# Kernel optimization log

Measured on AMD Instinct MI355X. Metric: run time of the kernel, lower is better.

## Reference

```python
import jax, jax.numpy as jnp
import numpy as np

H, W, C = 64, 64, 2048
IMG = 224


def setup_inputs() -> dict:
    key = jax.random.key(0)
    features = jax.random.normal(key, (2, H, W, C), dtype=jnp.float32)
    return {"features": features, "img_size": IMG}


def reference(features, img_size):
    # features: [2, H, W, C] -- query (index 0) and target (index 1) feature maps.
    x0 = features[0]  # [H, W, C]
    x1 = features[1]  # [H, W, C]
    # Correlation volume: Decomposition[i,j,k,l] = sum_c x0[i,j,c] * x1[k,l,c]
    # (replaces the quadruple Python loop with a single GEMM-shaped einsum)
    decom = jnp.einsum('ijc,klc->ijkl', x0, x1)  # [H, W, H, W]
    decom = decom / jnp.max(decom)
    # NOTE: source calls `Decomposition.clamp(min=0)` without assignment -> no-op.
    decom_1 = jnp.sum(decom, axis=(2, 3))  # [H, W] saliency on query image
    decom_2 = jnp.sum(decom, axis=(0, 1))  # [H, W] saliency on target image
    stacked = jnp.stack((decom_1, decom_2))  # [2, H, W]
    # F.interpolate(mode='bilinear', align_corners=False) == half-pixel bilinear resize
    out = jax.image.resize(stacked, (2, img_size, img_size), method='bilinear')
    return out  # [2, img_size, img_size]
```

## Files before the change

kernel.cpp:

```cpp
#include <hip/hip_runtime.h>
#include <hip/hip_bf16.h>

#define HW    4096
#define CDIM  2048
#define IMG   224
#define NTKI  64
#define NTM   128
#define LROW  528
#define QSCALE 21.166666f

typedef int   int4v  __attribute__((ext_vector_type(4)));
typedef int   i32x16 __attribute__((ext_vector_type(16)));
typedef char  char4v __attribute__((ext_vector_type(4)));

__device__ __forceinline__ i32x16 zi16() {
    i32x16 z;
#pragma unroll
    for (int i = 0; i < 16; ++i) z[i] = 0;
    return z;
}
__device__ __forceinline__ char quant8(float x) {
    int r = __float2int_rn(x * QSCALE);
    r = min(max(r, -127), 127);
    return (char)r;
}

__global__ __launch_bounds__(256) void convert_pack_colsum(
    const float* __restrict__ feat,
    char* __restrict__ Ap, char* __restrict__ Bp,
    float* __restrict__ s0, float* __restrict__ s1) {
    __shared__ char lds[32 * LROW];
    __shared__ float csum[512];
    const int tid = threadIdx.x;
    const int mat = blockIdx.z;
    const int tm  = blockIdx.y;
    const int kb0 = blockIdx.x * 512;
    const float* src = feat + (size_t)mat * HW * CDIM + (size_t)(tm * 32) * CDIM + kb0;

    const int cc = (tid & 127) * 4;
    float a0 = 0.f, a1 = 0.f, a2 = 0.f, a3 = 0.f;
#pragma unroll
    for (int j = 0; j < 16; ++j) {
        const int r = j * 2 + (tid >> 7);
        float4 v = *(const float4*)&src[(size_t)r * CDIM + cc];
        a0 += v.x; a1 += v.y; a2 += v.z; a3 += v.w;
        char4v q;
        q[0] = quant8(v.x); q[1] = quant8(v.y);
        q[2] = quant8(v.z); q[3] = quant8(v.w);
        *(char4v*)&lds[r * LROW + cc] = q;
    }
    if (tid >= 128) {
        csum[cc + 0] = a0; csum[cc + 1] = a1;
        csum[cc + 2] = a2; csum[cc + 3] = a3;
    }
    __syncthreads();
    if (tid < 128) {
        float* s = mat ? s1 : s0;
        atomicAdd(&s[kb0 + cc + 0], a0 + csum[cc + 0]);
        atomicAdd(&s[kb0 + cc + 1], a1 + csum[cc + 1]);
        atomicAdd(&s[kb0 + cc + 2], a2 + csum[cc + 2]);
        atomicAdd(&s[kb0 + cc + 3], a3 + csum[cc + 3]);
    }

    const int l = tid & 63, w = tid >> 6;
    char* dstbase = mat ? Bp : Ap;
#pragma unroll
    for (int i = 0; i < 4; ++i) {
        const int tkl = w * 4 + i;
        int4v v = *(const int4v*)&lds[(l & 31) * LROW + tkl * 32 + (l >> 5) * 16];
        const int tkg = blockIdx.x * 16 + tkl;
        *(int4v*)&dstbase[((size_t)(tm * NTKI + tkg) * 64 + l) * 16] = v;
    }
}

__global__ __launch_bounds__(256, 4) void gemm_max_kernel(
    const char* __restrict__ Ap, const char* __restrict__ Bp,
    float* __restrict__ blockmax) {
    const int tid  = threadIdx.x;
    const int lane = tid & 63;
    const int wave = tid >> 6;
    const int wm = wave >> 1, wn = wave & 1;
    const int bm = blockIdx.y, bn = blockIdx.x;

    const int tmA = bm * 4 + wm * 2;
    const int tnB = bn * 4 + wn * 2;
    const char* a0p = Ap + (size_t)(tmA * NTKI) * 1024 + lane * 16;
    const char* a1p = a0p + (size_t)NTKI * 1024;
    const char* b0p = Bp + (size_t)(tnB * NTKI) * 1024 + lane * 16;
    const char* b1p = b0p + (size_t)NTKI * 1024;

    i32x16 acc00 = zi16(), acc01 = zi16(), acc10 = zi16(), acc11 = zi16();

    int4v ca0 = *(const int4v*)a0p;
    int4v ca1 = *(const int4v*)a1p;
    int4v cb0 = *(const int4v*)b0p;
    int4v cb1 = *(const int4v*)b1p;

#pragma unroll 2
    for (int tk = 0; tk < NTKI - 1; ++tk) {
        const size_t o = (size_t)(tk + 1) * 1024;
        const int4v na0 = *(const int4v*)(a0p + o);
        const int4v na1 = *(const int4v*)(a1p + o);
        const int4v nb0 = *(const int4v*)(b0p + o);
        const int4v nb1 = *(const int4v*)(b1p + o);
        acc00 = __builtin_amdgcn_mfma_i32_32x32x32_i8(ca0, cb0, acc00, 0, 0, 0);
        acc01 = __builtin_amdgcn_mfma_i32_32x32x32_i8(ca0, cb1, acc01, 0, 0, 0);
        acc10 = __builtin_amdgcn_mfma_i32_32x32x32_i8(ca1, cb0, acc10, 0, 0, 0);
        acc11 = __builtin_amdgcn_mfma_i32_32x32x32_i8(ca1, cb1, acc11, 0, 0, 0);
        ca0 = na0; ca1 = na1; cb0 = nb0; cb1 = nb1;
    }
    acc00 = __builtin_amdgcn_mfma_i32_32x32x32_i8(ca0, cb0, acc00, 0, 0, 0);
    acc01 = __builtin_amdgcn_mfma_i32_32x32x32_i8(ca0, cb1, acc01, 0, 0, 0);
    acc10 = __builtin_amdgcn_mfma_i32_32x32x32_i8(ca1, cb0, acc10, 0, 0, 0);
    acc11 = __builtin_amdgcn_mfma_i32_32x32x32_i8(ca1, cb1, acc11, 0, 0, 0);

    int m = INT_MIN;
#pragma unroll
    for (int i = 0; i < 16; ++i) {
        m = max(m, acc00[i]); m = max(m, acc01[i]);
        m = max(m, acc10[i]); m = max(m, acc11[i]);
    }
#pragma unroll
    for (int off = 32; off; off >>= 1)
        m = max(m, __shfl_down(m, off));

    __shared__ int wred[4];
    if (lane == 0) wred[wave] = m;
    __syncthreads();
    if (tid == 0) {
        const int im = max(max(wred[0], wred[1]), max(wred[2], wred[3]));
        blockmax[blockIdx.y * gridDim.x + blockIdx.x] =
            (float)im * (1.0f / (QSCALE * QSCALE));
    }
}

__global__ __launch_bounds__(256) void saliency_kernel(
    const float* __restrict__ feat, const float* __restrict__ s0,
    const float* __restrict__ s1, float* __restrict__ sal) {
    const int tid = threadIdx.x, lane = tid & 63, wave = tid >> 6;
    const int g = blockIdx.x * 4 + wave;
    const float* x;
    const float* s;
    if (g < HW) { x = feat + (size_t)g * CDIM;                            s = s1; }
    else        { x = feat + (size_t)HW * CDIM + (size_t)(g - HW) * CDIM; s = s0; }
    float acc = 0.f;
#pragma unroll
    for (int it = 0; it < 8; ++it) {
        const int c0 = it * 256 + lane * 4;
        float4 v = *(const float4*)&x[c0];
        float4 w = *(const float4*)&s[c0];
        acc += v.x * w.x + v.y * w.y + v.z * w.z + v.w * w.w;
    }
#pragma unroll
    for (int off = 32; off; off >>= 1) acc += __shfl_down(acc, off);
    if (lane == 0) sal[g] = acc;
}

__global__ __launch_bounds__(256) void resize_kernel(
    const float* __restrict__ sal, const float* __restrict__ bmax,
    float* __restrict__ out) {
    __shared__ float w[4];
    __shared__ float rM;
    const int tid = threadIdx.x;
    float m = -3.4e38f;
    for (int i = tid; i < 1024; i += 256) m = fmaxf(m, bmax[i]);
#pragma unroll
    for (int off = 32; off; off >>= 1) m = fmaxf(m, __shfl_down(m, off));
    if ((tid & 63) == 0) w[tid >> 6] = m;
    __syncthreads();
    if (tid == 0)
        rM = 1.0f / fmaxf(fmaxf(w[0], w[1]), fmaxf(w[2], w[3]));
    __syncthreads();

    const int idx = blockIdx.x * 256 + tid;
    if (idx >= 2 * IMG * IMG) return;
    const int ch = idx / (IMG * IMG);
    const int rem = idx % (IMG * IMG);
    const int oy = rem / IMG, ox = rem % IMG;
    const float scale = 64.0f / (float)IMG;
    const float sy = ((float)oy + 0.5f) * scale - 0.5f;
    const float sx = ((float)ox + 0.5f) * scale - 0.5f;
    const float fy0 = floorf(sy), fx0 = floorf(sx);
    const float wy = sy - fy0, wx = sx - fx0;
    int y0 = (int)fy0, x0 = (int)fx0;
    int y1 = min(max(y0 + 1, 0), 63), x1 = min(max(x0 + 1, 0), 63);
    y0 = min(max(y0, 0), 63); x0 = min(max(x0, 0), 63);
    const float* p = sal + ch * HW;
    const float v00 = p[y0 * 64 + x0], v01 = p[y0 * 64 + x1];
    const float v10 = p[y1 * 64 + x0], v11 = p[y1 * 64 + x1];
    out[idx] = ((1.f - wy) * ((1.f - wx) * v00 + wx * v01) +
                wy * ((1.f - wx) * v10 + wx * v11)) * rM;
}

extern "C" void kernel_launch(void* const* d_in, const int* in_sizes, int n_in,
                              void* d_out, int out_size, void* d_ws, size_t ws_size,
                              hipStream_t stream) {
    const float* feat = (const float*)d_in[0];
    float* out = (float*)d_out;

    char* ws = (char*)d_ws;
    char* Ap = ws;
    char* Bp = ws + (size_t)8 * 1024 * 1024;
    float* s0   = (float*)(ws + (size_t)16 * 1024 * 1024);
    float* s1   = s0 + CDIM;
    float* bmax = s1 + CDIM;
    float* sal  = bmax + 1024;

    hipMemsetAsync(s0, 0, 2 * CDIM * sizeof(float), stream);

    convert_pack_colsum<<<dim3(4, 128, 2), 256, 0, stream>>>(feat, Ap, Bp, s0, s1);
    gemm_max_kernel<<<dim3(32, 32), 256, 0, stream>>>(Ap, Bp, bmax);
    saliency_kernel<<<2048, 256, 0, stream>>>(feat, s0, s1, sal);
    const int nout = 2 * IMG * IMG;
    resize_kernel<<<(nout + 255) / 256, 256, 0, stream>>>(sal, bmax, out);
}
```

Measured before the change: 161.9 us.

## Replace atomic column sums with partials reduced inside GEMM kernel, drop memset

The convert kernel now handles 64 rows per block and writes per-block partial column sums to a buffer instead of using float atomics. The final 64-way reduction of those partials is folded into 16 blocks of the GEMM kernel. This removes the memset launch and the atomic contention. In exchange it doubles LDS use per convert block, halves that grid, and adds serial reduction work to a few GEMM blocks.

```diff
diff --git a/kernel.cpp b/kernel.cpp
--- a/kernel.cpp
+++ b/kernel.cpp
@@ -25,22 +25,22 @@
     return (char)r;
 }
 
-__global__ __launch_bounds__(256) void convert_pack_colsum(
+__global__ __launch_bounds__(256) void convert_pack_partial(
     const float* __restrict__ feat,
     char* __restrict__ Ap, char* __restrict__ Bp,
-    float* __restrict__ s0, float* __restrict__ s1) {
-    __shared__ char lds[32 * LROW];
+    float* __restrict__ P) {
+    __shared__ char lds[64 * LROW];
     __shared__ float csum[512];
     const int tid = threadIdx.x;
     const int mat = blockIdx.z;
-    const int tm  = blockIdx.y;
+    const int rm  = blockIdx.y;
     const int kb0 = blockIdx.x * 512;
-    const float* src = feat + (size_t)mat * HW * CDIM + (size_t)(tm * 32) * CDIM + kb0;
+    const float* src = feat + (size_t)mat * HW * CDIM + (size_t)(rm * 64) * CDIM + kb0;
 
     const int cc = (tid & 127) * 4;
     float a0 = 0.f, a1 = 0.f, a2 = 0.f, a3 = 0.f;
 #pragma unroll
-    for (int j = 0; j < 16; ++j) {
+    for (int j = 0; j < 32; ++j) {
         const int r = j * 2 + (tid >> 7);
         float4 v = *(const float4*)&src[(size_t)r * CDIM + cc];
         a0 += v.x; a1 += v.y; a2 += v.z; a3 += v.w;
@@ -55,19 +55,21 @@
     }
     __syncthreads();
     if (tid < 128) {
-        float* s = mat ? s1 : s0;
-        atomicAdd(&s[kb0 + cc + 0], a0 + csum[cc + 0]);
-        atomicAdd(&s[kb0 + cc + 1], a1 + csum[cc + 1]);
-        atomicAdd(&s[kb0 + cc + 2], a2 + csum[cc + 2]);
-        atomicAdd(&s[kb0 + cc + 3], a3 + csum[cc + 3]);
+        float4 p;
+        p.x = a0 + csum[cc + 0]; p.y = a1 + csum[cc + 1];
+        p.z = a2 + csum[cc + 2]; p.w = a3 + csum[cc + 3];
+        *(float4*)&P[((size_t)mat * 64 + rm) * CDIM + kb0 + cc] = p;
     }
 
     const int l = tid & 63, w = tid >> 6;
     char* dstbase = mat ? Bp : Ap;
 #pragma unroll
-    for (int i = 0; i < 4; ++i) {
-        const int tkl = w * 4 + i;
-        int4v v = *(const int4v*)&lds[(l & 31) * LROW + tkl * 32 + (l >> 5) * 16];
+    for (int i = 0; i < 8; ++i) {
+        const int t = w * 8 + i;
+        const int tml = t >> 4, tkl = t & 15;
+        int4v v = *(const int4v*)
+            &lds[(tml * 32 + (l & 31)) * LROW + tkl * 32 + (l >> 5) * 16];
+        const int tm  = rm * 2 + tml;
         const int tkg = blockIdx.x * 16 + tkl;
         *(int4v*)&dstbase[((size_t)(tm * NTKI + tkg) * 64 + l) * 16] = v;
     }
@@ -75,12 +77,23 @@
 
 __global__ __launch_bounds__(256, 4) void gemm_max_kernel(
     const char* __restrict__ Ap, const char* __restrict__ Bp,
+    const float* __restrict__ P, float* __restrict__ s,
     float* __restrict__ blockmax) {
     const int tid  = threadIdx.x;
     const int lane = tid & 63;
     const int wave = tid >> 6;
     const int wm = wave >> 1, wn = wave & 1;
     const int bm = blockIdx.y, bn = blockIdx.x;
+
+    if (bm == 31 && bn < 16) {
+        const int mat = bn >> 3;
+        const int c = (bn & 7) * 256 + tid;
+        const float* Pp = P + (size_t)mat * 64 * CDIM + c;
+        float sum = 0.f;
+#pragma unroll 8
+        for (int r = 0; r < 64; ++r) sum += Pp[(size_t)r * CDIM];
+        s[mat * CDIM + c] = sum;
+    }
 
     const int tmA = bm * 4 + wm * 2;
     const int tnB = bn * 4 + wn * 2;
@@ -135,20 +148,20 @@
 }
 
 __global__ __launch_bounds__(256) void saliency_kernel(
-    const float* __restrict__ feat, const float* __restrict__ s0,
-    const float* __restrict__ s1, float* __restrict__ sal) {
+    const float* __restrict__ feat, const float* __restrict__ s,
+    float* __restrict__ sal) {
     const int tid = threadIdx.x, lane = tid & 63, wave = tid >> 6;
     const int g = blockIdx.x * 4 + wave;
     const float* x;
-    const float* s;
-    if (g < HW) { x = feat + (size_t)g * CDIM;                            s = s1; }
-    else        { x = feat + (size_t)HW * CDIM + (size_t)(g - HW) * CDIM; s = s0; }
+    const float* sv;
+    if (g < HW) { x = feat + (size_t)g * CDIM;                            sv = s + CDIM; }
+    else        { x = feat + (size_t)HW * CDIM + (size_t)(g - HW) * CDIM; sv = s; }
     float acc = 0.f;
 #pragma unroll
     for (int it = 0; it < 8; ++it) {
         const int c0 = it * 256 + lane * 4;
         float4 v = *(const float4*)&x[c0];
-        float4 w = *(const float4*)&s[c0];
+        float4 w = *(const float4*)&sv[c0];
         acc += v.x * w.x + v.y * w.y + v.z * w.z + v.w * w.w;
     }
 #pragma unroll
@@ -201,16 +214,14 @@
     char* ws = (char*)d_ws;
     char* Ap = ws;
     char* Bp = ws + (size_t)8 * 1024 * 1024;
-    float* s0   = (float*)(ws + (size_t)16 * 1024 * 1024);
-    float* s1   = s0 + CDIM;
-    float* bmax = s1 + CDIM;
+    float* P    = (float*)(ws + (size_t)16 * 1024 * 1024);
+    float* s    = P + 2 * 64 * CDIM;
+    float* bmax = s + 2 * CDIM;
     float* sal  = bmax + 1024;
 
-    hipMemsetAsync(s0, 0, 2 * CDIM * sizeof(float), stream);
-
-    convert_pack_colsum<<<dim3(4, 128, 2), 256, 0, stream>>>(feat, Ap, Bp, s0, s1);
-    gemm_max_kernel<<<dim3(32, 32), 256, 0, stream>>>(Ap, Bp, bmax);
-    saliency_kernel<<<2048, 256, 0, stream>>>(feat, s0, s1, sal);
+    convert_pack_partial<<<dim3(4, 64, 2), 256, 0, stream>>>(feat, Ap, Bp, P);
+    gemm_max_kernel<<<dim3(32, 32), 256, 0, stream>>>(Ap, Bp, P, s, bmax);
+    saliency_kernel<<<2048, 256, 0, stream>>>(feat, s, sal);
     const int nout = 2 * IMG * IMG;
     resize_kernel<<<(nout + 255) / 256, 256, 0, stream>>>(sal, bmax, out);
 }
```

New measurement: 146.7 us. 9.4% less time.
